# Optimization experiments

Hardware: AMD Instinct MI355X
Metric: run time of the kernel (lower is better)

Reference implementation:

```python
import jax, jax.numpy as jnp
import numpy as np

N = 8192
E = 262144
D_IN = 128
D_OUT = 128


def setup_inputs() -> dict:
    key = jax.random.key(0)
    k1, k2, k3, k4 = jax.random.split(key, 4)
    x = jax.random.normal(k1, (N, D_IN), dtype=jnp.float32)
    edge_index = jax.random.randint(k2, (2, E), 0, N, dtype=jnp.int64)
    # Linear(in_channels, out_channels) params (Kaiming-uniform-ish init scale)
    bound = 1.0 / np.sqrt(D_IN)
    W = jax.random.uniform(k3, (D_OUT, D_IN), minval=-bound, maxval=bound, dtype=jnp.float32)
    b = jax.random.uniform(k4, (D_OUT,), minval=-bound, maxval=bound, dtype=jnp.float32)
    return {"x": x, "edge_index": edge_index, "W": W, "b": b}


def reference(x, edge_index, W, b):
    num_nodes = x.shape[0]
    # Dense adjacency via scatter-set (duplicates collapse to 1, like torch assignment)
    adjacency = jnp.zeros((num_nodes, num_nodes), dtype=x.dtype)
    adjacency = adjacency.at[edge_index[0], edge_index[1]].set(1.0)
    adjacency = adjacency + jnp.eye(num_nodes, dtype=x.dtype)
    degree = adjacency.sum(axis=1, keepdims=True)  # [N,1]
    norm = jnp.where(degree > 0, degree ** -0.5, jnp.zeros_like(degree))
    norm = norm * norm.T  # [N,N] symmetric normalization
    norm = norm * adjacency
    h = x @ W.T + b  # [N, D_OUT]
    out = norm @ h
    return out
```

## Files before the change

kernel.cpp:

```cpp
#include <hip/hip_runtime.h>
#include <hip/hip_fp16.h>
#include <cstdint>
#include <cstddef>

#define NN 8192
#define DD 128
#define RCAP 96
#define NSCAT 1024

__global__ __launch_bounds__(256) void zero_kernel(uint4* __restrict__ p, int n4) {
    int i = blockIdx.x * blockDim.x + threadIdx.x;
    if (i < n4) p[i] = make_uint4(0u, 0u, 0u, 0u);
}

__global__ __launch_bounds__(64) void fused_linear_scatter(
    const float* __restrict__ x, const int* __restrict__ ei,
    const float* __restrict__ Wm, const float* __restrict__ bias,
    int* __restrict__ cnt, int* __restrict__ adj,
    __half* __restrict__ h, int E)
{
    const int bid = blockIdx.x;
    if (bid < NSCAT) {
        const int t = bid * 64 + threadIdx.x;
        const int4 sv = ((const int4*)ei)[t];
        const int4 dv = ((const int4*)(ei + E))[t];
        if ((unsigned)sv.x < (unsigned)NN && (unsigned)dv.x < (unsigned)NN) {
            int pos = atomicAdd(&cnt[sv.x], 1);
            if (pos < RCAP) adj[(size_t)sv.x * RCAP + pos] = dv.x;
        }
        if ((unsigned)sv.y < (unsigned)NN && (unsigned)dv.y < (unsigned)NN) {
            int pos = atomicAdd(&cnt[sv.y], 1);
            if (pos < RCAP) adj[(size_t)sv.y * RCAP + pos] = dv.y;
        }
        if ((unsigned)sv.z < (unsigned)NN && (unsigned)dv.z < (unsigned)NN) {
            int pos = atomicAdd(&cnt[sv.z], 1);
            if (pos < RCAP) adj[(size_t)sv.z * RCAP + pos] = dv.z;
        }
        if ((unsigned)sv.w < (unsigned)NN && (unsigned)dv.w < (unsigned)NN) {
            int pos = atomicAdd(&cnt[sv.w], 1);
            if (pos < RCAP) adj[(size_t)sv.w * RCAP + pos] = dv.w;
        }
        return;
    }

    __shared__ float Wl[32][36];
    __shared__ float xl[32][36];
    const int lb = bid - NSCAT;
    const int tid = threadIdx.x;
    const int row0 = (lb >> 2) * 32;
    const int c0   = (lb & 3) * 32;
    const int d4 = tid & 7;
    const int rg = tid >> 3;

    float acc[4][4];
    #pragma unroll
    for (int r = 0; r < 4; ++r)
        #pragma unroll
        for (int c = 0; c < 4; ++c) acc[r][c] = 0.0f;

    for (int kt = 0; kt < 4; ++kt) {
        #pragma unroll
        for (int i = tid; i < 1024; i += 64) {
            int o = i >> 5, kk = i & 31;
            Wl[kk][o] = Wm[(size_t)(c0 + o) * DD + kt * 32 + kk];
        }
        #pragma unroll
        for (int i = tid; i < 1024; i += 64) {
            int r = i >> 5, kk = i & 31;
            xl[kk][r] = x[(size_t)(row0 + r) * DD + kt * 32 + kk];
        }
        __syncthreads();
        #pragma unroll 8
        for (int kk = 0; kk < 32; ++kk) {
            const float4 w4 = *(const float4*)&Wl[kk][d4 * 4];
            const float4 x4 = *(const float4*)&xl[kk][rg * 4];
            acc[0][0] += x4.x * w4.x; acc[0][1] += x4.x * w4.y; acc[0][2] += x4.x * w4.z; acc[0][3] += x4.x * w4.w;
            acc[1][0] += x4.y * w4.x; acc[1][1] += x4.y * w4.y; acc[1][2] += x4.y * w4.z; acc[1][3] += x4.y * w4.w;
            acc[2][0] += x4.z * w4.x; acc[2][1] += x4.z * w4.y; acc[2][2] += x4.z * w4.z; acc[2][3] += x4.z * w4.w;
            acc[3][0] += x4.w * w4.x; acc[3][1] += x4.w * w4.y; acc[3][2] += x4.w * w4.z; acc[3][3] += x4.w * w4.w;
        }
        __syncthreads();
    }

    const float4 b4 = *(const float4*)&bias[c0 + d4 * 4];
    #pragma unroll
    for (int r = 0; r < 4; ++r) {
        const int row = row0 + rg * 4 + r;
        float4 o;
        o.x = acc[r][0] + b4.x;
        o.y = acc[r][1] + b4.y;
        o.z = acc[r][2] + b4.z;
        o.w = acc[r][3] + b4.w;
        union { uint2 u; __half2 hh[2]; } pk;
        pk.hh[0] = __floats2half2_rn(o.x, o.y);
        pk.hh[1] = __floats2half2_rn(o.z, o.w);
        *(uint2*)&h[(size_t)row * DD + c0 + d4 * 4] = pk.u;
    }
}

__global__ __launch_bounds__(256) void dedup_kernel(const int* __restrict__ cnt,
                                                    const int* __restrict__ adj,
                                                    int* __restrict__ uadj,
                                                    int* __restrict__ ucnt,
                                                    float* __restrict__ dinv) {
    __shared__ unsigned bm[4][256];
    const int tid = threadIdx.x;
    const int lane = tid & 63;
    const int wave = tid >> 6;
    const int row = blockIdx.x * 4 + wave;

    bm[wave][lane]       = 0u;
    bm[wave][lane + 64]  = 0u;
    bm[wave][lane + 128] = 0u;
    bm[wave][lane + 192] = 0u;
    __syncthreads();

    int rc = cnt[row]; if (rc > RCAP) rc = RCAP;
    for (int k = lane; k < rc; k += 64) {
        int dst = adj[(size_t)row * RCAP + k];
        atomicOr(&bm[wave][dst >> 5], 1u << (dst & 31));
    }
    __syncthreads();

    unsigned w0 = bm[wave][lane * 4 + 0];
    unsigned w1 = bm[wave][lane * 4 + 1];
    unsigned w2 = bm[wave][lane * 4 + 2];
    unsigned w3 = bm[wave][lane * 4 + 3];
    int c = __popc(w0) + __popc(w1) + __popc(w2) + __popc(w3);
    int scan = c;
    #pragma unroll
    for (int off = 1; off < 64; off <<= 1) {
        int o = __shfl_up(scan, off);
        if (lane >= off) scan += o;
    }
    int pos = row * RCAP + (scan - c);
    const int b0 = lane * 128;
    unsigned ws[4] = {w0, w1, w2, w3};
    #pragma unroll
    for (int q = 0; q < 4; ++q) {
        unsigned w = ws[q];
        while (w) {
            int bb = __ffs(w) - 1;
            w &= w - 1;
            uadj[pos++] = b0 + q * 32 + bb;
        }
    }
    if (lane == 63) {
        ucnt[row] = scan;
        dinv[row] = rsqrtf((float)(scan + 1));
    }
}

__global__ __launch_bounds__(256) void agg_kernel(const int* __restrict__ ucnt,
                                                  const int* __restrict__ uadj,
                                                  const float* __restrict__ dinv,
                                                  const __half* __restrict__ h,
                                                  float* __restrict__ out) {
    const int lane = threadIdx.x & 63;
    const int wave = threadIdx.x >> 6;
    const int row = blockIdx.x * 4 + wave;
    const int u = ucnt[row];

    int nl0 = 0, nl1 = 0;
    float nd0 = 0.f, nd1 = 0.f;
    if (lane < u) { nl0 = uadj[(size_t)row * RCAP + lane]; nd0 = dinv[nl0]; }
    const int u1 = u - 64;
    if (lane < u1) { nl1 = uadj[(size_t)row * RCAP + 64 + lane]; nd1 = dinv[nl1]; }

    const __half2* h2 = (const __half2*)h;
    float2 a0 = make_float2(0.f, 0.f);
    float2 a1 = make_float2(0.f, 0.f);
    float2 a2 = make_float2(0.f, 0.f);
    float2 a3 = make_float2(0.f, 0.f);

    const int kmax = (u < 64) ? u : 64;
    int k = 0;
    for (; k + 3 < kmax; k += 4) {
        int j0 = __shfl(nl0, k),     j1 = __shfl(nl0, k + 1);
        int j2 = __shfl(nl0, k + 2), j3 = __shfl(nl0, k + 3);
        float s0 = __shfl(nd0, k),     s1 = __shfl(nd0, k + 1);
        float s2 = __shfl(nd0, k + 2), s3 = __shfl(nd0, k + 3);
        float2 v0 = __half22float2(h2[(size_t)j0 * 64 + lane]);
        float2 v1 = __half22float2(h2[(size_t)j1 * 64 + lane]);
        float2 v2 = __half22float2(h2[(size_t)j2 * 64 + lane]);
        float2 v3 = __half22float2(h2[(size_t)j3 * 64 + lane]);
        a0.x += s0 * v0.x; a0.y += s0 * v0.y;
        a1.x += s1 * v1.x; a1.y += s1 * v1.y;
        a2.x += s2 * v2.x; a2.y += s2 * v2.y;
        a3.x += s3 * v3.x; a3.y += s3 * v3.y;
    }
    for (; k < kmax; ++k) {
        int j0 = __shfl(nl0, k);
        float s0 = __shfl(nd0, k);
        float2 v0 = __half22float2(h2[(size_t)j0 * 64 + lane]);
        a0.x += s0 * v0.x; a0.y += s0 * v0.y;
    }
    for (k = 64; k < u; ++k) {
        int j0 = __shfl(nl1, k - 64);
        float s0 = __shfl(nd1, k - 64);
        float2 v0 = __half22float2(h2[(size_t)j0 * 64 + lane]);
        a0.x += s0 * v0.x; a0.y += s0 * v0.y;
    }

    float2 acc;
    acc.x = (a0.x + a1.x) + (a2.x + a3.x);
    acc.y = (a0.y + a1.y) + (a2.y + a3.y);
    const float di = dinv[row];
    float2 hv = __half22float2(h2[(size_t)row * 64 + lane]);
    float2 o;
    o.x = di * (acc.x + di * hv.x);
    o.y = di * (acc.y + di * hv.y);
    *(float2*)&out[(size_t)row * DD + lane * 2] = o;
}

extern "C" void kernel_launch(void* const* d_in, const int* in_sizes, int n_in,
                              void* d_out, int out_size, void* d_ws, size_t ws_size,
                              hipStream_t stream) {
    const float* x  = (const float*)d_in[0];
    const int*   ei = (const int*)d_in[1];
    const float* Wm = (const float*)d_in[2];
    const float* bs = (const float*)d_in[3];
    float* out = (float*)d_out;
    const int E = in_sizes[1] / 2;

    char* p = (char*)d_ws;
    int* cnt    = (int*)p;   p += (size_t)NN * sizeof(int);
    int* ucnt   = (int*)p;   p += (size_t)NN * sizeof(int);
    float* dinv = (float*)p; p += (size_t)NN * sizeof(float);
    int* adj    = (int*)p;   p += (size_t)NN * RCAP * sizeof(int);
    int* uadj   = (int*)p;   p += (size_t)NN * RCAP * sizeof(int);
    __half* h   = (__half*)p;

    const int n4 = (NN * (int)sizeof(int)) / 16;
    zero_kernel<<<8, 256, 0, stream>>>((uint4*)cnt, n4);
    fused_linear_scatter<<<NSCAT + 1024, 64, 0, stream>>>(x, ei, Wm, bs, cnt, adj, h, E);
    dedup_kernel<<<NN / 4, 256, 0, stream>>>(cnt, adj, uadj, ucnt, dinv);
    agg_kernel<<<NN / 4, 256, 0, stream>>>(ucnt, uadj, dinv, h, out);
}
```

Before: 43.45 us.

## Use 256-thread blocks with split-K across waves in fused linear/scatter kernel

Widens the fused scatter+linear kernel from 64 to 256 threads per block. Scatter blocks now each handle 4x more edges, so there are fewer of them. Linear blocks load the full K=128 slice into shared memory at once and split K across the four waves, then combine the partial sums with a shared-memory tree reduction. This targets the serial K-loop of small blocks and gives more waves per block to hide latency. The cost is a larger shared-memory footprint (about 36KB per block), which may lower occupancy, plus extra barriers for the reduction.

```diff
diff --git a/kernel.cpp b/kernel.cpp
--- a/kernel.cpp
+++ b/kernel.cpp
@@ -6,22 +6,26 @@
 #define NN 8192
 #define DD 128
 #define RCAP 96
-#define NSCAT 1024
+#define NSCAT 256
 
 __global__ __launch_bounds__(256) void zero_kernel(uint4* __restrict__ p, int n4) {
     int i = blockIdx.x * blockDim.x + threadIdx.x;
     if (i < n4) p[i] = make_uint4(0u, 0u, 0u, 0u);
 }
 
-__global__ __launch_bounds__(64) void fused_linear_scatter(
+__global__ __launch_bounds__(256) void fused_linear_scatter(
     const float* __restrict__ x, const int* __restrict__ ei,
     const float* __restrict__ Wm, const float* __restrict__ bias,
     int* __restrict__ cnt, int* __restrict__ adj,
     __half* __restrict__ h, int E)
 {
+    __shared__ float Wl[128][36];
+    __shared__ float xl[128][36];
     const int bid = blockIdx.x;
+    const int tid = threadIdx.x;
+
     if (bid < NSCAT) {
-        const int t = bid * 64 + threadIdx.x;
+        const int t = bid * 256 + tid;
         const int4 sv = ((const int4*)ei)[t];
         const int4 dv = ((const int4*)(ei + E))[t];
         if ((unsigned)sv.x < (unsigned)NN && (unsigned)dv.x < (unsigned)NN) {
@@ -43,14 +47,25 @@
         return;
     }
 
-    __shared__ float Wl[32][36];
-    __shared__ float xl[32][36];
     const int lb = bid - NSCAT;
-    const int tid = threadIdx.x;
     const int row0 = (lb >> 2) * 32;
     const int c0   = (lb & 3) * 32;
-    const int d4 = tid & 7;
-    const int rg = tid >> 3;
+    const int wave = tid >> 6;
+    const int lane = tid & 63;
+    const int d4 = lane & 7;
+    const int rg = lane >> 3;
+
+    #pragma unroll
+    for (int i = tid; i < 4096; i += 256) {
+        int o = i >> 7, kk = i & 127;
+        Wl[kk][o] = Wm[(size_t)(c0 + o) * DD + kk];
+    }
+    #pragma unroll
+    for (int i = tid; i < 4096; i += 256) {
+        int r = i >> 7, kk = i & 127;
+        xl[kk][r] = x[(size_t)(row0 + r) * DD + kk];
+    }
+    __syncthreads();
 
     float acc[4][4];
     #pragma unroll
@@ -58,43 +73,63 @@
         #pragma unroll
         for (int c = 0; c < 4; ++c) acc[r][c] = 0.0f;
 
-    for (int kt = 0; kt < 4; ++kt) {
-        #pragma unroll
-        for (int i = tid; i < 1024; i += 64) {
-            int o = i >> 5, kk = i & 31;
-            Wl[kk][o] = Wm[(size_t)(c0 + o) * DD + kt * 32 + kk];
-        }
-        #pragma unroll
-        for (int i = tid; i < 1024; i += 64) {
-            int r = i >> 5, kk = i & 31;
-            xl[kk][r] = x[(size_t)(row0 + r) * DD + kt * 32 + kk];
-        }
-        __syncthreads();
-        #pragma unroll 8
-        for (int kk = 0; kk < 32; ++kk) {
-            const float4 w4 = *(const float4*)&Wl[kk][d4 * 4];
-            const float4 x4 = *(const float4*)&xl[kk][rg * 4];
-            acc[0][0] += x4.x * w4.x; acc[0][1] += x4.x * w4.y; acc[0][2] += x4.x * w4.z; acc[0][3] += x4.x * w4.w;
-            acc[1][0] += x4.y * w4.x; acc[1][1] += x4.y * w4.y; acc[1][2] += x4.y * w4.z; acc[1][3] += x4.y * w4.w;
-            acc[2][0] += x4.z * w4.x; acc[2][1] += x4.z * w4.y; acc[2][2] += x4.z * w4.z; acc[2][3] += x4.z * w4.w;
-            acc[3][0] += x4.w * w4.x; acc[3][1] += x4.w * w4.y; acc[3][2] += x4.w * w4.z; acc[3][3] += x4.w * w4.w;
-        }
-        __syncthreads();
-    }
-
-    const float4 b4 = *(const float4*)&bias[c0 + d4 * 4];
-    #pragma unroll
-    for (int r = 0; r < 4; ++r) {
-        const int row = row0 + rg * 4 + r;
-        float4 o;
-        o.x = acc[r][0] + b4.x;
-        o.y = acc[r][1] + b4.y;
-        o.z = acc[r][2] + b4.z;
-        o.w = acc[r][3] + b4.w;
-        union { uint2 u; __half2 hh[2]; } pk;
-        pk.hh[0] = __floats2half2_rn(o.x, o.y);
-        pk.hh[1] = __floats2half2_rn(o.z, o.w);
-        *(uint2*)&h[(size_t)row * DD + c0 + d4 * 4] = pk.u;
+    #pragma unroll 8
+    for (int j = 0; j < 32; ++j) {
+        const int kk = wave * 32 + j;
+        const float4 w4 = *(const float4*)&Wl[kk][d4 * 4];
+        const float4 x4 = *(const float4*)&xl[kk][rg * 4];
+        acc[0][0] += x4.x * w4.x; acc[0][1] += x4.x * w4.y; acc[0][2] += x4.x * w4.z; acc[0][3] += x4.x * w4.w;
+        acc[1][0] += x4.y * w4.x; acc[1][1] += x4.y * w4.y; acc[1][2] += x4.y * w4.z; acc[1][3] += x4.y * w4.w;
+        acc[2][0] += x4.z * w4.x; acc[2][1] += x4.z * w4.y; acc[2][2] += x4.z * w4.z; acc[2][3] += x4.z * w4.w;
+        acc[3][0] += x4.w * w4.x; acc[3][1] += x4.w * w4.y; acc[3][2] += x4.w * w4.z; acc[3][3] += x4.w * w4.w;
+    }
+    __syncthreads();
+
+    float4* buf0 = (float4*)&Wl[0][0];
+    float4* buf1 = (float4*)&xl[0][0];
+    if (wave == 2) {
+        #pragma unroll
+        for (int r = 0; r < 4; ++r) buf0[lane * 17 + r] = make_float4(acc[r][0], acc[r][1], acc[r][2], acc[r][3]);
+    } else if (wave == 3) {
+        #pragma unroll
+        for (int r = 0; r < 4; ++r) buf1[lane * 17 + r] = make_float4(acc[r][0], acc[r][1], acc[r][2], acc[r][3]);
+    }
+    __syncthreads();
+    if (wave == 0) {
+        #pragma unroll
+        for (int r = 0; r < 4; ++r) {
+            float4 v = buf0[lane * 17 + r];
+            acc[r][0] += v.x; acc[r][1] += v.y; acc[r][2] += v.z; acc[r][3] += v.w;
+        }
+    } else if (wave == 1) {
+        #pragma unroll
+        for (int r = 0; r < 4; ++r) {
+            float4 v = buf1[lane * 17 + r];
+            acc[r][0] += v.x; acc[r][1] += v.y; acc[r][2] += v.z; acc[r][3] += v.w;
+        }
+    }
+    __syncthreads();
+    if (wave == 1) {
+        #pragma unroll
+        for (int r = 0; r < 4; ++r) buf0[lane * 17 + r] = make_float4(acc[r][0], acc[r][1], acc[r][2], acc[r][3]);
+    }
+    __syncthreads();
+    if (wave == 0) {
+        const float4 b4 = *(const float4*)&bias[c0 + d4 * 4];
+        #pragma unroll
+        for (int r = 0; r < 4; ++r) {
+            float4 v = buf0[lane * 17 + r];
+            const int row = row0 + rg * 4 + r;
+            float4 o;
+            o.x = acc[r][0] + v.x + b4.x;
+            o.y = acc[r][1] + v.y + b4.y;
+            o.z = acc[r][2] + v.z + b4.z;
+            o.w = acc[r][3] + v.w + b4.w;
+            union { uint2 u; __half2 hh[2]; } pk;
+            pk.hh[0] = __floats2half2_rn(o.x, o.y);
+            pk.hh[1] = __floats2half2_rn(o.z, o.w);
+            *(uint2*)&h[(size_t)row * DD + c0 + d4 * 4] = pk.u;
+        }
     }
 }
 
@@ -233,7 +268,7 @@
 
     const int n4 = (NN * (int)sizeof(int)) / 16;
     zero_kernel<<<8, 256, 0, stream>>>((uint4*)cnt, n4);
-    fused_linear_scatter<<<NSCAT + 1024, 64, 0, stream>>>(x, ei, Wm, bs, cnt, adj, h, E);
+    fused_linear_scatter<<<NSCAT + 1024, 256, 0, stream>>>(x, ei, Wm, bs, cnt, adj, h, E);
     dedup_kernel<<<NN / 4, 256, 0, stream>>>(cnt, adj, uadj, ucnt, dinv);
     agg_kernel<<<NN / 4, 256, 0, stream>>>(ucnt, uadj, dinv, h, out);
 }
```

Result: slower. 45.04 us (+3.7%).
